# Kernel optimization log

Measured on AMD Instinct MI355X. Metric: run time of the kernel, lower is better.

The kernel has to match this reference:

```python
import jax, jax.numpy as jnp
import numpy as np

# dims
P = 16            # patch size
IMG = 224
D = 768           # embed dim
DEPTH = 12
DI = 1536         # d_inner = expand * D
N = 16            # d_state
DCONV = 4
DTR = 48          # dt_rank = ceil(D / 16)
GS = IMG // P     # 14
L = GS * GS       # 196
KEEP = 49         # (1 - 0.75) * 196
EPS = 1e-5


def _pos2d(embed_dim, gs):
    # replicates get_2d_sincos_pos_embed (numpy, fp32)
    def emb1(ed, pos):
        omega = np.arange(ed // 2, dtype=np.float32) / (ed / 2.0)
        omega = 1.0 / 10000 ** omega
        out = np.einsum('m,d->md', pos.reshape(-1).astype(np.float32), omega)
        return np.concatenate([np.sin(out), np.cos(out)], axis=1)
    gh = np.arange(gs, dtype=np.float32)
    grid = np.meshgrid(gh, gh)  # (w, h) per source
    return np.concatenate([emb1(embed_dim // 2, grid[0]), emb1(embed_dim // 2, grid[1])], axis=1)


def _ln(x, w, b):
    mu = x.mean(-1, keepdims=True)
    var = ((x - mu) ** 2).mean(-1, keepdims=True)
    return (x - mu) * jax.lax.rsqrt(var + EPS) * w + b


def setup_inputs() -> dict:
    key = jax.random.key(0)
    ks = jax.random.split(key, 12)
    s = 0.02
    dt = jnp.exp(jax.random.uniform(ks[7], (DEPTH, DI)) * (np.log(0.1) - np.log(0.001)) + np.log(0.001))
    return {
        'imgs': jax.random.normal(ks[0], (8, 3, IMG, IMG), jnp.float32),
        'noise': jax.random.uniform(ks[1], (8, L), jnp.float32),
        'patch_w': s * jax.random.normal(ks[2], (D, 3, P, P), jnp.float32),
        'patch_b': jnp.zeros((D,), jnp.float32),
        'pos_embed': jnp.asarray(_pos2d(D, GS), jnp.float32),            # [L, D]
        'ln_w': jnp.ones((DEPTH, D), jnp.float32),
        'ln_b': jnp.zeros((DEPTH, D), jnp.float32),
        'in_proj_w': s * jax.random.normal(ks[3], (DEPTH, 2 * DI, D), jnp.float32),
        'conv_w': 0.1 * jax.random.normal(ks[4], (DEPTH, DI, 1, DCONV), jnp.float32),
        'conv_b': jnp.zeros((DEPTH, DI), jnp.float32),
        'x_proj_w': s * jax.random.normal(ks[5], (DEPTH, DTR + 2 * N, DI), jnp.float32),
        'dt_w': s * jax.random.normal(ks[6], (DEPTH, DI, DTR), jnp.float32),
        'dt_b': jnp.log(jnp.expm1(dt)),                                   # inverse softplus
        'A_log': jnp.broadcast_to(jnp.log(jnp.arange(1, N + 1, dtype=jnp.float32)), (DEPTH, DI, N)).copy(),
        'D_skip': jnp.ones((DEPTH, DI), jnp.float32),
        'ssm_ln_w': jnp.ones((DEPTH, DI), jnp.float32),
        'ssm_ln_b': jnp.zeros((DEPTH, DI), jnp.float32),
        'out_proj_w': s * jax.random.normal(ks[8], (DEPTH, D, DI), jnp.float32),
        'final_ln_w': jnp.ones((D,), jnp.float32),
        'final_ln_b': jnp.zeros((D,), jnp.float32),
    }


def _encoder(imgs, noise, patch_w, patch_b, pos_embed, ln_w, ln_b, in_proj_w, conv_w,
             conv_b, x_proj_w, dt_w, dt_b, A_log, D_skip, ssm_ln_w, ssm_ln_b,
             out_proj_w, final_ln_w, final_ln_b):
    B = imgs.shape[0]
    # patch embed: conv stride=kernel=P -> [B, D, 14, 14] -> [B, L, D]
    x = jax.lax.conv_general_dilated(imgs, patch_w, (P, P), 'VALID',
                                     dimension_numbers=('NCHW', 'OIHW', 'NCHW'))
    x = (x + patch_b[None, :, None, None]).reshape(B, D, L).transpose(0, 2, 1)
    x = x + pos_embed[None]

    # random masking (MAE): keep KEEP tokens per sample
    ids_shuffle = jnp.argsort(noise, axis=1)
    ids_restore = jnp.argsort(ids_shuffle, axis=1)
    ids_keep = ids_shuffle[:, :KEEP]
    x = jnp.take_along_axis(x, ids_keep[:, :, None], axis=1)  # [B, KEEP, D]
    mask = jnp.ones((B, L), jnp.float32).at[:, :KEEP].set(0.0)
    mask = jnp.take_along_axis(mask, ids_restore, axis=1)

    def block_step(carry, lp):
        hs, res = carry
        lnw, lnb, ipw, cw, cb, xpw, dtw, dtb, alog, dsk, slw, slb, opw = lp
        res = res + hs                       # Add
        h = _ln(res, lnw, lnb)               # LN
        # --- Mamba mixer ---
        xz = h @ ipw.T                       # [B,K,2*DI]
        xi, z = jnp.split(xz, 2, axis=-1)
        xc = xi.transpose(0, 2, 1)           # [B,DI,K]
        xc = jnp.pad(xc, ((0, 0), (0, 0), (DCONV - 1, 0)))  # causal depthwise conv
        xc = jax.lax.conv_general_dilated(xc, cw, (1,), 'VALID',
                                          dimension_numbers=('NCH', 'OIH', 'NCH'),
                                          feature_group_count=DI)
        xc = jax.nn.silu(xc + cb[None, :, None]).transpose(0, 2, 1)  # [B,K,DI]
        xdbl = xc @ xpw.T                    # [B,K,DTR+2N]
        dtr, Bm, Cm = jnp.split(xdbl, [DTR, DTR + N], axis=-1)
        dt = jax.nn.softplus(dtr @ dtw.T + dtb)      # [B,K,DI]
        A = -jnp.exp(alog)                            # [DI,N]
        dA = jnp.exp(dt[..., None] * A)               # [B,K,DI,N]
        dBx = (dt * xc)[..., None] * Bm[:, :, None, :]
        def scan_step(hstate, inp):
            dA_t, dBx_t, C_t = inp
            hstate = dA_t * hstate + dBx_t            # [B,DI,N]
            y = jnp.einsum('bdn,bn->bd', hstate, C_t)
            return hstate, y
        h0 = jnp.zeros((xc.shape[0], DI, N), xc.dtype)
        _, ys = jax.lax.scan(scan_step, h0,
                             (dA.transpose(1, 0, 2, 3), dBx.transpose(1, 0, 2, 3), Cm.transpose(1, 0, 2)))
        y = ys.transpose(1, 0, 2) + dsk * xc          # D skip
        y = _ln(y, slw, slb)                           # norm after SSM
        y = y * jax.nn.silu(z)                         # gate
        out = y @ opw.T                                # [B,K,D]
        return (out, res), None

    res0 = jnp.zeros_like(x)
    (hs, res), _ = jax.lax.scan(block_step, (x, res0),
                                (ln_w, ln_b, in_proj_w, conv_w, conv_b, x_proj_w, dt_w,
                                 dt_b, A_log, D_skip, ssm_ln_w, ssm_ln_b, out_proj_w))
    latent = _ln(res + hs, final_ln_w, final_ln_b)
    return latent, mask, ids_restore


def reference(imgs, noise, patch_w, patch_b, pos_embed, ln_w, ln_b, in_proj_w, conv_w,
              conv_b, x_proj_w, dt_w, dt_b, A_log, D_skip, ssm_ln_w, ssm_ln_b,
              out_proj_w, final_ln_w, final_ln_b):
    return _encoder(imgs, noise, patch_w, patch_b, pos_embed, ln_w, ln_b, in_proj_w,
                    conv_w, conv_b, x_proj_w, dt_w, dt_b, A_log, D_skip, ssm_ln_w,
                    ssm_ln_b, out_proj_w, final_ln_w, final_ln_b)
```

## Files before the change

### kernel.cpp

```cpp
#include <hip/hip_runtime.h>
#include <cstdint>
#include <cstddef>

namespace {

constexpr int kD    = 768;
constexpr int kDI   = 1536;
constexpr int kN    = 16;
constexpr int kDTR  = 48;
constexpr int kL    = 196;
constexpr int kKeep = 49;
constexpr int kB    = 8;
constexpr int kTok  = kB * kKeep;
constexpr int kPatchRows = kB * kL;
constexpr float kEps = 1e-5f;

typedef __attribute__((ext_vector_type(8))) short short8;
typedef __attribute__((ext_vector_type(4))) float f32x4;

__device__ __forceinline__ short f2bf(float f) {
  unsigned u = __float_as_uint(f);
  return (short)((u + 0x7FFFu + ((u >> 16) & 1u)) >> 16);
}

__device__ __forceinline__ short8 pack8(float4 a, float4 b) {
  short8 r;
  r[0] = f2bf(a.x); r[1] = f2bf(a.y); r[2] = f2bf(a.z); r[3] = f2bf(a.w);
  r[4] = f2bf(b.x); r[5] = f2bf(b.y); r[6] = f2bf(b.z); r[7] = f2bf(b.w);
  return r;
}

__device__ __forceinline__ float block_sum256(float x, float* sbuf) {
#pragma unroll
  for (int o = 32; o > 0; o >>= 1) x += __shfl_down(x, o, 64);
  int wid = threadIdx.x >> 6;
  if ((threadIdx.x & 63) == 0) sbuf[wid] = x;
  __syncthreads();
  float r = sbuf[0] + sbuf[1] + sbuf[2] + sbuf[3];
  __syncthreads();
  return r;
}

__global__ __launch_bounds__(256) void im2col_kernel(const float* __restrict__ imgs,
                                                     float* __restrict__ A2) {
  int idx = blockIdx.x * 256 + threadIdx.x;
  if (idx >= kPatchRows * kD) return;
  int col = idx % kD;
  int row = idx / kD;
  int b = row / kL, l = row % kL;
  int gy = l / 14, gx = l % 14;
  int c   = col >> 8;
  int rem = col & 255;
  int py = rem >> 4, px = rem & 15;
  A2[idx] = imgs[((b * 3 + c) * 224 + gy * 16 + py) * 224 + gx * 16 + px];
}

template <int SPLIT, int ACT, bool KG>
__global__ __launch_bounds__(256) void gemm_mfma(const float* __restrict__ A, int lda,
                                                 const float* __restrict__ W,
                                                 const float* __restrict__ bias,
                                                 float* __restrict__ C, int ldc,
                                                 int M, int N, int K) {
  __shared__ __align__(16) short As[8][64][8];
  __shared__ __align__(16) short Bs[8][64][8];
  const int tid = threadIdx.x;
  const int bm = blockIdx.x * 64;
  const int bn = blockIdx.y * 64;
  const int kc = K / SPLIT;
  const int k0 = blockIdx.z * kc;
  const int nk = (kc + 63) / 64;
  const int sr = tid >> 2;
  const int sq = tid & 3;
  const int lane = tid & 63;
  const int wm = ((tid >> 6) >> 1) * 32;
  const int wn = ((tid >> 6) & 1) * 32;
  const bool mok = (bm + sr) < M;
  const bool nok = (bn + sr) < N;
  const float* Ap = A + (size_t)(bm + sr) * lda + k0 + sq * 16;
  const float* Wp = W + (size_t)(bn + sr) * K + k0 + sq * 16;

  f32x4 acc[2][2];
#pragma unroll
  for (int i = 0; i < 2; ++i)
#pragma unroll
    for (int j = 0; j < 2; ++j) acc[i][j] = (f32x4){0.f, 0.f, 0.f, 0.f};

  for (int kt = 0; kt < nk; ++kt) {
    const int kb = kt * 64;
    const float4 z4 = make_float4(0.f, 0.f, 0.f, 0.f);
    float4 a0 = z4, a1 = z4, a2 = z4, a3 = z4;
    float4 w0 = z4, w1 = z4, w2 = z4, w3 = z4;
    const float* ap = Ap + kb;
    const float* wp = Wp + kb;
    if (!KG) {
      if (mok) {
        a0 = *(const float4*)ap;       a1 = *(const float4*)(ap + 4);
        a2 = *(const float4*)(ap + 8); a3 = *(const float4*)(ap + 12);
      }
      if (nok) {
        w0 = *(const float4*)wp;       w1 = *(const float4*)(wp + 4);
        w2 = *(const float4*)(wp + 8); w3 = *(const float4*)(wp + 12);
      }
    } else {
      const int kq = k0 + kb + sq * 16;
      if (mok) {
        if (kq + 4  <= K) a0 = *(const float4*)ap;
        if (kq + 8  <= K) a1 = *(const float4*)(ap + 4);
        if (kq + 12 <= K) a2 = *(const float4*)(ap + 8);
        if (kq + 16 <= K) a3 = *(const float4*)(ap + 12);
      }
      if (nok) {
        if (kq + 4  <= K) w0 = *(const float4*)wp;
        if (kq + 8  <= K) w1 = *(const float4*)(wp + 4);
        if (kq + 12 <= K) w2 = *(const float4*)(wp + 8);
        if (kq + 16 <= K) w3 = *(const float4*)(wp + 12);
      }
    }
    if (kt) __syncthreads();
    *(short8*)&As[sq * 2][sr][0]     = pack8(a0, a1);
    *(short8*)&As[sq * 2 + 1][sr][0] = pack8(a2, a3);
    *(short8*)&Bs[sq * 2][sr][0]     = pack8(w0, w1);
    *(short8*)&Bs[sq * 2 + 1][sr][0] = pack8(w2, w3);
    __syncthreads();
#pragma unroll
    for (int kh = 0; kh < 2; ++kh) {
      const int kg = kh * 4 + (lane >> 4);
      short8 af0 = *(const short8*)&As[kg][wm + (lane & 15)][0];
      short8 af1 = *(const short8*)&As[kg][wm + 16 + (lane & 15)][0];
      short8 bf0 = *(const short8*)&Bs[kg][wn + (lane & 15)][0];
      short8 bf1 = *(const short8*)&Bs[kg][wn + 16 + (lane & 15)][0];
      acc[0][0] = __builtin_amdgcn_mfma_f32_16x16x32_bf16(af0, bf0, acc[0][0], 0, 0, 0);
      acc[0][1] = __builtin_amdgcn_mfma_f32_16x16x32_bf16(af0, bf1, acc[0][1], 0, 0, 0);
      acc[1][0] = __builtin_amdgcn_mfma_f32_16x16x32_bf16(af1, bf0, acc[1][0], 0, 0, 0);
      acc[1][1] = __builtin_amdgcn_mfma_f32_16x16x32_bf16(af1, bf1, acc[1][1], 0, 0, 0);
    }
  }

  const int mrow = (lane >> 4) * 4;
  const int ncol = lane & 15;
#pragma unroll
  for (int i2 = 0; i2 < 2; ++i2)
#pragma unroll
    for (int j2 = 0; j2 < 2; ++j2) {
      int n = bn + wn + j2 * 16 + ncol;
      if (n >= N) continue;
      float bv = 0.f;
      if (SPLIT == 1) bv = bias ? bias[n] : 0.f;
#pragma unroll
      for (int r = 0; r < 4; ++r) {
        int m = bm + wm + i2 * 16 + mrow + r;
        if (m >= M) continue;
        float v = acc[i2][j2][r];
        if (SPLIT == 1) {
          v += bv;
          if (ACT == 1) v = (v > 20.f) ? v : log1pf(expf(v));
          C[(size_t)m * ldc + n] = v;
        } else {
          C[(size_t)blockIdx.z * ((size_t)M * N) + (size_t)m * N + n] = v;
        }
      }
    }
}

__global__ __launch_bounds__(256) void reduce_kernel(const float* __restrict__ part,
                                                     float* __restrict__ out,
                                                     int total4, int Z) {
  int i = blockIdx.x * 256 + threadIdx.x;
  if (i >= total4) return;
  const float4* p = (const float4*)part;
  float4 s = p[i];
  for (int z = 1; z < Z; ++z) {
    float4 v = p[(size_t)z * total4 + i];
    s.x += v.x; s.y += v.y; s.z += v.z; s.w += v.w;
  }
  ((float4*)out)[i] = s;
}

__global__ __launch_bounds__(256) void sort_kernel(const float* __restrict__ noise,
                                                   int* __restrict__ ids_keep,
                                                   float* __restrict__ mask_out,
                                                   float* __restrict__ idsr_out) {
  __shared__ float nb[kL];
  int b = blockIdx.x;
  int t = threadIdx.x;
  if (t < kL) nb[t] = noise[b * kL + t];
  __syncthreads();
  if (t < kL) {
    float v = nb[t];
    int rank = 0;
    for (int j = 0; j < kL; ++j) {
      float u = nb[j];
      rank += (u < v || (u == v && j < t)) ? 1 : 0;
    }
    if (rank < kKeep) ids_keep[b * kKeep + rank] = t;
    idsr_out[b * kL + t] = (float)rank;
    mask_out[b * kL + t] = (rank < kKeep) ? 0.f : 1.f;
  }
}

__global__ __launch_bounds__(256) void gather_kernel(const float* __restrict__ x0,
                                                     const int* __restrict__ ids_keep,
                                                     const float* __restrict__ pos,
                                                     float* __restrict__ hs) {
  int m = blockIdx.x;
  int b = m / kKeep, k = m % kKeep;
  int l = ids_keep[b * kKeep + k];
  const float* src = x0 + (size_t)(b * kL + l) * kD;
  const float* pp  = pos + (size_t)l * kD;
  float* dst = hs + (size_t)m * kD;
  for (int d = threadIdx.x; d < kD; d += 256) dst[d] = src[d] + pp[d];
}

template <int DD>
__global__ __launch_bounds__(256) void add_ln_kernel(const float* __restrict__ hs,
                                                     float* __restrict__ res,
                                                     const float* __restrict__ w,
                                                     const float* __restrict__ b,
                                                     float* __restrict__ out) {
  constexpr int PT = DD / 256;
  __shared__ float sbuf[4];
  int m = blockIdx.x;
  int t = threadIdx.x;
  float v[PT];
  float s = 0.f;
#pragma unroll
  for (int i = 0; i < PT; ++i) {
    int d = t + i * 256;
    v[i] = res[(size_t)m * DD + d] + hs[(size_t)m * DD + d];
    s += v[i];
  }
  float mean = block_sum256(s, sbuf) * (1.f / DD);
  float s2 = 0.f;
#pragma unroll
  for (int i = 0; i < PT; ++i) { float d0 = v[i] - mean; s2 += d0 * d0; }
  float var = block_sum256(s2, sbuf) * (1.f / DD);
  float rstd = rsqrtf(var + kEps);
#pragma unroll
  for (int i = 0; i < PT; ++i) {
    int d = t + i * 256;
    res[(size_t)m * DD + d] = v[i];
    out[(size_t)m * DD + d] = (v[i] - mean) * rstd * w[d] + b[d];
  }
}

__global__ __launch_bounds__(256) void conv_silu_kernel(const float* __restrict__ xz,
                                                        const float* __restrict__ cw,
                                                        const float* __restrict__ cb,
                                                        float* __restrict__ xc) {
  int idx = blockIdx.x * 256 + threadIdx.x;
  if (idx >= kTok * kDI) return;
  int d  = idx % kDI;
  int mt = idx / kDI;
  int t = mt % kKeep;
  int b = mt / kKeep;
  float acc = cb[d];
#pragma unroll
  for (int k = 0; k < 4; ++k) {
    int tt = t - 3 + k;
    if (tt >= 0) acc += xz[(size_t)(b * kKeep + tt) * 3072 + d] * cw[d * 4 + k];
  }
  xc[idx] = acc / (1.f + expf(-acc));
}

__global__ __launch_bounds__(64) void scan_kernel(const float* __restrict__ dt,
                                                  const float* __restrict__ xc,
                                                  const float* __restrict__ xdbl,
                                                  const float* __restrict__ A_log,
                                                  const float* __restrict__ D_skip,
                                                  float* __restrict__ y) {
  __shared__ float bcs[kKeep][32];
  int d = blockIdx.x * 64 + threadIdx.x;
  int b = blockIdx.y;
  for (int i = threadIdx.x; i < kKeep * 32; i += 64) {
    int t = i >> 5, n = i & 31;
    bcs[t][n] = xdbl[(size_t)(b * kKeep + t) * 80 + kDTR + n];
  }
  __syncthreads();
  float Aloc[kN];
#pragma unroll
  for (int n = 0; n < kN; ++n) Aloc[n] = -expf(A_log[d * kN + n]);
  float dsk = D_skip[d];
  float s[kN];
#pragma unroll
  for (int n = 0; n < kN; ++n) s[n] = 0.f;

  size_t base = (size_t)(b * kKeep) * kDI + d;
  float dtv = dt[base];
  float xcv = xc[base];
  for (int t = 0; t < kKeep; ++t) {
    float dtn = 0.f, xcn = 0.f;
    if (t + 1 < kKeep) {
      dtn = dt[base + (size_t)(t + 1) * kDI];
      xcn = xc[base + (size_t)(t + 1) * kDI];
    }
    float dx = dtv * xcv;
    float yv = 0.f;
#pragma unroll
    for (int n = 0; n < kN; ++n) {
      float sn = expf(dtv * Aloc[n]) * s[n] + dx * bcs[t][n];
      s[n] = sn;
      yv += sn * bcs[t][16 + n];
    }
    y[base + (size_t)t * kDI] = yv + dsk * xcv;
    dtv = dtn; xcv = xcn;
  }
}

__global__ __launch_bounds__(256) void ssm_ln_silu_kernel(const float* __restrict__ y,
                                                          const float* __restrict__ xz,
                                                          const float* __restrict__ w,
                                                          const float* __restrict__ b,
                                                          float* __restrict__ y2) {
  constexpr int PT = kDI / 256;
  __shared__ float sbuf[4];
  int m = blockIdx.x;
  int t = threadIdx.x;
  float v[PT];
  float s = 0.f;
#pragma unroll
  for (int i = 0; i < PT; ++i) {
    int d = t + i * 256;
    v[i] = y[(size_t)m * kDI + d];
    s += v[i];
  }
  float mean = block_sum256(s, sbuf) * (1.f / kDI);
  float s2 = 0.f;
#pragma unroll
  for (int i = 0; i < PT; ++i) { float d0 = v[i] - mean; s2 += d0 * d0; }
  float var = block_sum256(s2, sbuf) * (1.f / kDI);
  float rstd = rsqrtf(var + kEps);
#pragma unroll
  for (int i = 0; i < PT; ++i) {
    int d = t + i * 256;
    float z = xz[(size_t)m * 3072 + kDI + d];
    y2[(size_t)m * kDI + d] =
        ((v[i] - mean) * rstd * w[d] + b[d]) * (z / (1.f + expf(-z)));
  }
}

}

extern "C" void kernel_launch(void* const* d_in, const int* in_sizes, int n_in,
                              void* d_out, int out_size, void* d_ws, size_t ws_size,
                              hipStream_t stream) {
  const float* imgs       = (const float*)d_in[0];
  const float* noise      = (const float*)d_in[1];
  const float* patch_w    = (const float*)d_in[2];
  const float* patch_b    = (const float*)d_in[3];
  const float* pos_embed  = (const float*)d_in[4];
  const float* ln_w       = (const float*)d_in[5];
  const float* ln_b       = (const float*)d_in[6];
  const float* in_proj_w  = (const float*)d_in[7];
  const float* conv_w     = (const float*)d_in[8];
  const float* conv_b     = (const float*)d_in[9];
  const float* x_proj_w   = (const float*)d_in[10];
  const float* dt_w       = (const float*)d_in[11];
  const float* dt_b       = (const float*)d_in[12];
  const float* A_log      = (const float*)d_in[13];
  const float* D_skip     = (const float*)d_in[14];
  const float* ssm_ln_w   = (const float*)d_in[15];
  const float* ssm_ln_b   = (const float*)d_in[16];
  const float* out_proj_w = (const float*)d_in[17];
  const float* final_ln_w = (const float*)d_in[18];
  const float* final_ln_b = (const float*)d_in[19];

  float* out      = (float*)d_out;
  float* latent   = out;
  float* mask_out = out + 301056;
  float* idsr_out = out + 301056 + 1568;

  float* ws   = (float*)d_ws;
  float* hs   = ws;
  float* res  = hs   + 301056;
  float* h    = res  + 301056;
  float* xz   = h    + 301056;
  float* xc   = xz   + 1204224;
  float* xdbl = xc   + 602112;
  float* dtb_ = xdbl + 31360;
  float* ybuf = dtb_ + 602112;
  float* y2   = ybuf + 602112;
  int*   ids_keep = (int*)(y2 + 602112);
  float* A2 = xz;
  float* x0 = xc;
  float* part_xdbl = ybuf;
  float* part_out  = dtb_;

  {
    int tot = kPatchRows * kD;
    im2col_kernel<<<(tot + 255) / 256, 256, 0, stream>>>(imgs, A2);
    gemm_mfma<1, 0, false><<<dim3(25, 12, 1), 256, 0, stream>>>(
        A2, kD, patch_w, patch_b, x0, kD, kPatchRows, kD, kD);
  }

  sort_kernel<<<kB, 256, 0, stream>>>(noise, ids_keep, mask_out, idsr_out);

  gather_kernel<<<kTok, 256, 0, stream>>>(x0, ids_keep, pos_embed, hs);

  hipMemsetAsync(res, 0, (size_t)kTok * kD * sizeof(float), stream);

  for (int l = 0; l < 12; ++l) {
    const float* lnw  = ln_w  + (size_t)l * kD;
    const float* lnb  = ln_b  + (size_t)l * kD;
    const float* ipw  = in_proj_w  + (size_t)l * 2 * kDI * kD;
    const float* cw   = conv_w     + (size_t)l * kDI * 4;
    const float* cb   = conv_b     + (size_t)l * kDI;
    const float* xpw  = x_proj_w   + (size_t)l * (kDTR + 2 * kN) * kDI;
    const float* dtw  = dt_w       + (size_t)l * kDI * kDTR;
    const float* dtbv = dt_b       + (size_t)l * kDI;
    const float* alog = A_log      + (size_t)l * kDI * kN;
    const float* dsk  = D_skip     + (size_t)l * kDI;
    const float* slw  = ssm_ln_w   + (size_t)l * kDI;
    const float* slb  = ssm_ln_b   + (size_t)l * kDI;
    const float* opw  = out_proj_w + (size_t)l * kD * kDI;

    add_ln_kernel<kD><<<kTok, 256, 0, stream>>>(hs, res, lnw, lnb, h);

    gemm_mfma<1, 0, false><<<dim3(7, 48, 1), 256, 0, stream>>>(
        h, kD, ipw, nullptr, xz, 2 * kDI, kTok, 2 * kDI, kD);

    conv_silu_kernel<<<(kTok * kDI + 255) / 256, 256, 0, stream>>>(xz, cw, cb, xc);

    gemm_mfma<24, 0, false><<<dim3(7, 2, 24), 256, 0, stream>>>(
        xc, kDI, xpw, nullptr, part_xdbl, 80, kTok, 80, kDI);
    reduce_kernel<<<(7840 + 255) / 256, 256, 0, stream>>>(part_xdbl, xdbl, 7840, 24);

    gemm_mfma<1, 1, true><<<dim3(7, 24, 1), 256, 0, stream>>>(
        xdbl, 80, dtw, dtbv, dtb_, kDI, kTok, kDI, kDTR);

    scan_kernel<<<dim3(24, kB), 64, 0, stream>>>(dtb_, xc, xdbl, alog, dsk, ybuf);

    ssm_ln_silu_kernel<<<kTok, 256, 0, stream>>>(ybuf, xz, slw, slb, y2);

    gemm_mfma<4, 0, false><<<dim3(7, 12, 4), 256, 0, stream>>>(
        y2, kDI, opw, nullptr, part_out, kD, kTok, kD, kDI);
    reduce_kernel<<<(75264 + 255) / 256, 256, 0, stream>>>(part_out, hs, 75264, 4);
  }

  add_ln_kernel<kD><<<kTok, 256, 0, stream>>>(hs, res, final_ln_w, final_ln_b,
                                              latent);
}
```

Before: 1.600 ms.

## Fuse conv+SiLU into x_proj GEMM, dt_proj into scan, reduce into add-LN

Removes the standalone depthwise conv kernel by recomputing conv+SiLU while loading the x_proj GEMM A tile, and recomputes it again inside the scan. The dt projection and softplus now run per timestep inside the scan kernel, reading dt weights from registers. The out_proj split-K partial sums are reduced inside the next add+LayerNorm instead of a separate reduce kernel. This cuts about three launches per layer and the xc/dt intermediate buffers, at the cost of redundant conv work and heavier per-thread scan work.

```diff
diff --git a/kernel.cpp b/kernel.cpp
--- a/kernel.cpp
+++ b/kernel.cpp
@@ -29,6 +29,8 @@
   r[4] = f2bf(b.x); r[5] = f2bf(b.y); r[6] = f2bf(b.z); r[7] = f2bf(b.w);
   return r;
 }
+
+__device__ __forceinline__ float silu(float x) { return x / (1.f + expf(-x)); }
 
 __device__ __forceinline__ float block_sum256(float x, float* sbuf) {
 #pragma unroll
@@ -55,7 +57,7 @@
   A2[idx] = imgs[((b * 3 + c) * 224 + gy * 16 + py) * 224 + gx * 16 + px];
 }
 
-template <int SPLIT, int ACT, bool KG>
+template <int SPLIT>
 __global__ __launch_bounds__(256) void gemm_mfma(const float* __restrict__ A, int lda,
                                                  const float* __restrict__ W,
                                                  const float* __restrict__ bias,
@@ -68,7 +70,7 @@
   const int bn = blockIdx.y * 64;
   const int kc = K / SPLIT;
   const int k0 = blockIdx.z * kc;
-  const int nk = (kc + 63) / 64;
+  const int nk = kc / 64;
   const int sr = tid >> 2;
   const int sq = tid & 3;
   const int lane = tid & 63;
@@ -92,29 +94,13 @@
     float4 w0 = z4, w1 = z4, w2 = z4, w3 = z4;
     const float* ap = Ap + kb;
     const float* wp = Wp + kb;
-    if (!KG) {
-      if (mok) {
-        a0 = *(const float4*)ap;       a1 = *(const float4*)(ap + 4);
-        a2 = *(const float4*)(ap + 8); a3 = *(const float4*)(ap + 12);
-      }
-      if (nok) {
-        w0 = *(const float4*)wp;       w1 = *(const float4*)(wp + 4);
-        w2 = *(const float4*)(wp + 8); w3 = *(const float4*)(wp + 12);
-      }
-    } else {
-      const int kq = k0 + kb + sq * 16;
-      if (mok) {
-        if (kq + 4  <= K) a0 = *(const float4*)ap;
-        if (kq + 8  <= K) a1 = *(const float4*)(ap + 4);
-        if (kq + 12 <= K) a2 = *(const float4*)(ap + 8);
-        if (kq + 16 <= K) a3 = *(const float4*)(ap + 12);
-      }
-      if (nok) {
-        if (kq + 4  <= K) w0 = *(const float4*)wp;
-        if (kq + 8  <= K) w1 = *(const float4*)(wp + 4);
-        if (kq + 12 <= K) w2 = *(const float4*)(wp + 8);
-        if (kq + 16 <= K) w3 = *(const float4*)(wp + 12);
-      }
+    if (mok) {
+      a0 = *(const float4*)ap;       a1 = *(const float4*)(ap + 4);
+      a2 = *(const float4*)(ap + 8); a3 = *(const float4*)(ap + 12);
+    }
+    if (nok) {
+      w0 = *(const float4*)wp;       w1 = *(const float4*)(wp + 4);
+      w2 = *(const float4*)(wp + 8); w3 = *(const float4*)(wp + 12);
     }
     if (kt) __syncthreads();
     *(short8*)&As[sq * 2][sr][0]     = pack8(a0, a1);
@@ -144,20 +130,117 @@
     for (int j2 = 0; j2 < 2; ++j2) {
       int n = bn + wn + j2 * 16 + ncol;
       if (n >= N) continue;
-      float bv = 0.f;
-      if (SPLIT == 1) bv = bias ? bias[n] : 0.f;
+      float bv = (SPLIT == 1 && bias) ? bias[n] : 0.f;
 #pragma unroll
       for (int r = 0; r < 4; ++r) {
         int m = bm + wm + i2 * 16 + mrow + r;
         if (m >= M) continue;
         float v = acc[i2][j2][r];
         if (SPLIT == 1) {
-          v += bv;
-          if (ACT == 1) v = (v > 20.f) ? v : log1pf(expf(v));
-          C[(size_t)m * ldc + n] = v;
+          C[(size_t)m * ldc + n] = v + bv;
         } else {
           C[(size_t)blockIdx.z * ((size_t)M * N) + (size_t)m * N + n] = v;
         }
+      }
+    }
+}
+
+__global__ __launch_bounds__(256) void gemm_xdbl_conv(const float* __restrict__ xz,
+                                                      const float* __restrict__ cw,
+                                                      const float* __restrict__ cb,
+                                                      const float* __restrict__ W,
+                                                      float* __restrict__ Cpart) {
+  __shared__ __align__(16) short As[8][64][8];
+  __shared__ __align__(16) short Bs[8][64][8];
+  const int tid = threadIdx.x;
+  const int bm = blockIdx.x * 64;
+  const int bn = blockIdx.y * 64;
+  const int k0 = blockIdx.z * 64;
+  const int sr = tid >> 2;
+  const int sq = tid & 3;
+  const int lane = tid & 63;
+  const int wm = ((tid >> 6) >> 1) * 32;
+  const int wn = ((tid >> 6) & 1) * 32;
+  const int m = bm + sr;
+  const bool mok = m < kTok;
+  const bool nok = (bn + sr) < 80;
+  const float4 z4 = make_float4(0.f, 0.f, 0.f, 0.f);
+
+  float4 a[4] = {z4, z4, z4, z4};
+  if (mok) {
+    const int b = m / kKeep, t = m % kKeep;
+    const int dbase = k0 + sq * 16;
+#pragma unroll
+    for (int g = 0; g < 4; ++g) {
+      const int d = dbase + g * 4;
+      float4 cacc = *(const float4*)&cb[d];
+      float4 c0 = *(const float4*)&cw[(d + 0) * 4];
+      float4 c1 = *(const float4*)&cw[(d + 1) * 4];
+      float4 c2 = *(const float4*)&cw[(d + 2) * 4];
+      float4 c3 = *(const float4*)&cw[(d + 3) * 4];
+      const float t0[4] = {c0.x, c0.y, c0.z, c0.w};
+      const float t1[4] = {c1.x, c1.y, c1.z, c1.w};
+      const float t2[4] = {c2.x, c2.y, c2.z, c2.w};
+      const float t3[4] = {c3.x, c3.y, c3.z, c3.w};
+#pragma unroll
+      for (int j = 0; j < 4; ++j) {
+        int tt = t - 3 + j;
+        if (tt < 0) continue;
+        float4 xv = *(const float4*)&xz[(size_t)(b * kKeep + tt) * 3072 + d];
+        cacc.x += xv.x * t0[j];
+        cacc.y += xv.y * t1[j];
+        cacc.z += xv.z * t2[j];
+        cacc.w += xv.w * t3[j];
+      }
+      cacc.x = silu(cacc.x); cacc.y = silu(cacc.y);
+      cacc.z = silu(cacc.z); cacc.w = silu(cacc.w);
+      a[g] = cacc;
+    }
+  }
+  float4 w0 = z4, w1 = z4, w2 = z4, w3 = z4;
+  if (nok) {
+    const float* wp = W + (size_t)(bn + sr) * kDI + k0 + sq * 16;
+    w0 = *(const float4*)wp;       w1 = *(const float4*)(wp + 4);
+    w2 = *(const float4*)(wp + 8); w3 = *(const float4*)(wp + 12);
+  }
+  *(short8*)&As[sq * 2][sr][0]     = pack8(a[0], a[1]);
+  *(short8*)&As[sq * 2 + 1][sr][0] = pack8(a[2], a[3]);
+  *(short8*)&Bs[sq * 2][sr][0]     = pack8(w0, w1);
+  *(short8*)&Bs[sq * 2 + 1][sr][0] = pack8(w2, w3);
+  __syncthreads();
+
+  f32x4 acc[2][2];
+#pragma unroll
+  for (int i = 0; i < 2; ++i)
+#pragma unroll
+    for (int j = 0; j < 2; ++j) acc[i][j] = (f32x4){0.f, 0.f, 0.f, 0.f};
+#pragma unroll
+  for (int kh = 0; kh < 2; ++kh) {
+    const int kg = kh * 4 + (lane >> 4);
+    short8 af0 = *(const short8*)&As[kg][wm + (lane & 15)][0];
+    short8 af1 = *(const short8*)&As[kg][wm + 16 + (lane & 15)][0];
+    short8 bf0 = *(const short8*)&Bs[kg][wn + (lane & 15)][0];
+    short8 bf1 = *(const short8*)&Bs[kg][wn + 16 + (lane & 15)][0];
+    acc[0][0] = __builtin_amdgcn_mfma_f32_16x16x32_bf16(af0, bf0, acc[0][0], 0, 0, 0);
+    acc[0][1] = __builtin_amdgcn_mfma_f32_16x16x32_bf16(af0, bf1, acc[0][1], 0, 0, 0);
+    acc[1][0] = __builtin_amdgcn_mfma_f32_16x16x32_bf16(af1, bf0, acc[1][0], 0, 0, 0);
+    acc[1][1] = __builtin_amdgcn_mfma_f32_16x16x32_bf16(af1, bf1, acc[1][1], 0, 0, 0);
+  }
+
+  const int mrow = (lane >> 4) * 4;
+  const int ncol = lane & 15;
+#pragma unroll
+  for (int i2 = 0; i2 < 2; ++i2)
+#pragma unroll
+    for (int j2 = 0; j2 < 2; ++j2) {
+      int n = bn + wn + j2 * 16 + ncol;
+      if (n >= 80) continue;
+#pragma unroll
+      for (int r = 0; r < 4; ++r) {
+        int mm = bm + wm + i2 * 16 + mrow + r;
+        if (mm >= kTok) continue;
+        Cpart[(size_t)blockIdx.z * (kTok * 80) + (size_t)mm * 80 + n] =
+            acc[i2][j2][r];
       }
     }
 }
@@ -211,8 +294,8 @@
   for (int d = threadIdx.x; d < kD; d += 256) dst[d] = src[d] + pp[d];
 }
 
-template <int DD>
-__global__ __launch_bounds__(256) void add_ln_kernel(const float* __restrict__ hs,
+template <int DD, int NP>
+__global__ __launch_bounds__(256) void add_ln_kernel(const float* __restrict__ part,
                                                      float* __restrict__ res,
                                                      const float* __restrict__ w,
                                                      const float* __restrict__ b,
@@ -226,8 +309,12 @@
 #pragma unroll
   for (int i = 0; i < PT; ++i) {
     int d = t + i * 256;
-    v[i] = res[(size_t)m * DD + d] + hs[(size_t)m * DD + d];
-    s += v[i];
+    float acc = res[(size_t)m * DD + d];
+#pragma unroll
+    for (int z = 0; z < NP; ++z)
+      acc += part[(size_t)z * (kTok * DD) + (size_t)m * DD + d];
+    v[i] = acc;
+    s += acc;
   }
   float mean = block_sum256(s, sbuf) * (1.f / DD);
   float s2 = 0.f;
@@ -243,66 +330,72 @@
   }
 }
 
-__global__ __launch_bounds__(256) void conv_silu_kernel(const float* __restrict__ xz,
-                                                        const float* __restrict__ cw,
-                                                        const float* __restrict__ cb,
-                                                        float* __restrict__ xc) {
-  int idx = blockIdx.x * 256 + threadIdx.x;
-  if (idx >= kTok * kDI) return;
-  int d  = idx % kDI;
-  int mt = idx / kDI;
-  int t = mt % kKeep;
-  int b = mt / kKeep;
-  float acc = cb[d];
-#pragma unroll
-  for (int k = 0; k < 4; ++k) {
-    int tt = t - 3 + k;
-    if (tt >= 0) acc += xz[(size_t)(b * kKeep + tt) * 3072 + d] * cw[d * 4 + k];
-  }
-  xc[idx] = acc / (1.f + expf(-acc));
-}
-
-__global__ __launch_bounds__(64) void scan_kernel(const float* __restrict__ dt,
-                                                  const float* __restrict__ xc,
-                                                  const float* __restrict__ xdbl,
-                                                  const float* __restrict__ A_log,
-                                                  const float* __restrict__ D_skip,
-                                                  float* __restrict__ y) {
+__global__ __launch_bounds__(64) void scan_dt_kernel(const float* __restrict__ xz,
+                                                     const float* __restrict__ xdbl,
+                                                     const float* __restrict__ cw,
+                                                     const float* __restrict__ cb,
+                                                     const float* __restrict__ dtw,
+                                                     const float* __restrict__ dtbv,
+                                                     const float* __restrict__ A_log,
+                                                     const float* __restrict__ D_skip,
+                                                     float* __restrict__ y) {
+  __shared__ __align__(16) float dtr_s[kKeep][kDTR];
   __shared__ float bcs[kKeep][32];
-  int d = blockIdx.x * 64 + threadIdx.x;
-  int b = blockIdx.y;
-  for (int i = threadIdx.x; i < kKeep * 32; i += 64) {
-    int t = i >> 5, n = i & 31;
-    bcs[t][n] = xdbl[(size_t)(b * kKeep + t) * 80 + kDTR + n];
+  const int d0 = blockIdx.x * 64;
+  const int b  = blockIdx.y;
+  const int t  = threadIdx.x;
+  for (int i = t; i < kKeep * 80; i += 64) {
+    int tt = i / 80, c = i % 80;
+    float v = xdbl[(size_t)(b * kKeep + tt) * 80 + c];
+    if (c < kDTR) dtr_s[tt][c] = v;
+    else bcs[tt][c - kDTR] = v;
   }
   __syncthreads();
+
+  const int d = d0 + t;
+  float4 wreg[12];
+#pragma unroll
+  for (int q = 0; q < 12; ++q)
+    wreg[q] = *(const float4*)&dtw[(size_t)d * kDTR + q * 4];
   float Aloc[kN];
 #pragma unroll
-  for (int n = 0; n < kN; ++n) Aloc[n] = -expf(A_log[d * kN + n]);
-  float dsk = D_skip[d];
+  for (int n = 0; n < kN; ++n) Aloc[n] = -expf(A_log[(size_t)d * kN + n]);
+  const float dsk = D_skip[d];
+  const float dtb0 = dtbv[d];
+  const float4 cw4 = *(const float4*)&cw[d * 4];
+  const float cb0 = cb[d];
+
   float s[kN];
 #pragma unroll
   for (int n = 0; n < kN; ++n) s[n] = 0.f;
-
-  size_t base = (size_t)(b * kKeep) * kDI + d;
-  float dtv = dt[base];
-  float xcv = xc[base];
-  for (int t = 0; t < kKeep; ++t) {
-    float dtn = 0.f, xcn = 0.f;
-    if (t + 1 < kKeep) {
-      dtn = dt[base + (size_t)(t + 1) * kDI];
-      xcn = xc[base + (size_t)(t + 1) * kDI];
-    }
+  float w0 = 0.f, w1 = 0.f, w2 = 0.f;
+
+  for (int tt = 0; tt < kKeep; ++tt) {
+    float xin = xz[(size_t)(b * kKeep + tt) * 3072 + d];
+    float cacc = cb0 + w0 * cw4.x + w1 * cw4.y + w2 * cw4.z + xin * cw4.w;
+    w0 = w1; w1 = w2; w2 = xin;
+    float xcv = silu(cacc);
+    float dacc = dtb0;
+#pragma unroll
+    for (int q = 0; q < 12; ++q) {
+      float4 r4 = *(const float4*)&dtr_s[tt][q * 4];
+      dacc += r4.x * wreg[q].x + r4.y * wreg[q].y +
+              r4.z * wreg[q].z + r4.w * wreg[q].w;
+    }
+    float dtv = (dacc > 20.f) ? dacc : log1pf(expf(dacc));
     float dx = dtv * xcv;
+    float4 bc[8];
+#pragma unroll
+    for (int q = 0; q < 8; ++q) bc[q] = *(const float4*)&bcs[tt][q * 4];
+    const float* bf = (const float*)&bc[0];
     float yv = 0.f;
 #pragma unroll
     for (int n = 0; n < kN; ++n) {
-      float sn = expf(dtv * Aloc[n]) * s[n] + dx * bcs[t][n];
+      float sn = expf(dtv * Aloc[n]) * s[n] + dx * bf[n];
       s[n] = sn;
-      yv += sn * bcs[t][16 + n];
-    }
-    y[base + (size_t)t * kDI] = yv + dsk * xcv;
-    dtv = dtn; xcv = xcn;
+      yv += sn * bf[16 + n];
+    }
+    y[(size_t)(b * kKeep + tt) * kDI + d] = yv + dsk * xcv;
   }
 }
 
@@ -334,7 +427,7 @@
     int d = t + i * 256;
     float z = xz[(size_t)m * 3072 + kDI + d];
     y2[(size_t)m * kDI + d] =
-        ((v[i] - mean) * rstd * w[d] + b[d]) * (z / (1.f + expf(-z)));
+        ((v[i] - mean) * rstd * w[d] + b[d]) * silu(z);
   }
 }
 
@@ -369,26 +462,24 @@
   float* mask_out = out + 301056;
   float* idsr_out = out + 301056 + 1568;
 
-  float* ws   = (float*)d_ws;
-  float* hs   = ws;
-  float* res  = hs   + 301056;
-  float* h    = res  + 301056;
-  float* xz   = h    + 301056;
-  float* xc   = xz   + 1204224;
-  float* xdbl = xc   + 602112;
-  float* dtb_ = xdbl + 31360;
-  float* ybuf = dtb_ + 602112;
-  float* y2   = ybuf + 602112;
-  int*   ids_keep = (int*)(y2 + 602112);
+  float* ws        = (float*)d_ws;
+  float* hs        = ws;
+  float* res       = hs + 301056;
+  float* h         = res + 301056;
+  float* xz        = h + 301056;
+  float* xdbl      = xz + 1204224;
+  float* part_xdbl = xdbl + 31360;
+  float* part_out  = part_xdbl + 752640;
+  float* ybuf      = part_out + 1204224;
+  float* y2        = ybuf + 602112;
+  int*   ids_keep  = (int*)(y2 + 602112);
   float* A2 = xz;
-  float* x0 = xc;
-  float* part_xdbl = ybuf;
-  float* part_out  = dtb_;
+  float* x0 = part_xdbl;
 
   {
     int tot = kPatchRows * kD;
     im2col_kernel<<<(tot + 255) / 256, 256, 0, stream>>>(imgs, A2);
-    gemm_mfma<1, 0, false><<<dim3(25, 12, 1), 256, 0, stream>>>(
+    gemm_mfma<1><<<dim3(25, 12, 1), 256, 0, stream>>>(
         A2, kD, patch_w, patch_b, x0, kD, kPatchRows, kD, kD);
   }
 
@@ -413,29 +504,26 @@
     const float* slb  = ssm_ln_b   + (size_t)l * kDI;
     const float* opw  = out_proj_w + (size_t)l * kD * kDI;
 
-    add_ln_kernel<kD><<<kTok, 256, 0, stream>>>(hs, res, lnw, lnb, h);
-
-    gemm_mfma<1, 0, false><<<dim3(7, 48, 1), 256, 0, stream>>>(
+    if (l == 0)
+      add_ln_kernel<kD, 1><<<kTok, 256, 0, stream>>>(hs, res, lnw, lnb, h);
+    else
+      add_ln_kernel<kD, 4><<<kTok, 256, 0, stream>>>(part_out, res, lnw, lnb, h);
+
+    gemm_mfma<1><<<dim3(7, 48, 1), 256, 0, stream>>>(
         h, kD, ipw, nullptr, xz, 2 * kDI, kTok, 2 * kDI, kD);
 
-    conv_silu_kernel<<<(kTok * kDI + 255) / 256, 256, 0, stream>>>(xz, cw, cb, xc);
-
-    gemm_mfma<24, 0, false><<<dim3(7, 2, 24), 256, 0, stream>>>(
-        xc, kDI, xpw, nullptr, part_xdbl, 80, kTok, 80, kDI);
+    gemm_xdbl_conv<<<dim3(7, 2, 24), 256, 0, stream>>>(xz, cw, cb, xpw, part_xdbl);
     reduce_kernel<<<(7840 + 255) / 256, 256, 0, stream>>>(part_xdbl, xdbl, 7840, 24);
 
-    gemm_mfma<1, 1, true><<<dim3(7, 24, 1), 256, 0, stream>>>(
-        xdbl, 80, dtw, dtbv, dtb_, kDI, kTok, kDI, kDTR);
-
-    scan_kernel<<<dim3(24, kB), 64, 0, stream>>>(dtb_, xc, xdbl, alog, dsk, ybuf);
+    scan_dt_kernel<<<dim3(24, kB), 64, 0, stream>>>(xz, xdbl, cw, cb, dtw, dtbv,
+                                                    alog, dsk, ybuf);
 
     ssm_ln_silu_kernel<<<kTok, 256, 0, stream>>>(ybuf, xz, slw, slb, y2);
 
-    gemm_mfma<4, 0, false><<<dim3(7, 12, 4), 256, 0, stream>>>(
+    gemm_mfma<4><<<dim3(7, 12, 4), 256, 0, stream>>>(
         y2, kDI, opw, nullptr, part_out, kD, kTok, kD, kDI);
-    reduce_kernel<<<(75264 + 255) / 256, 256, 0, stream>>>(part_out, hs, 75264, 4);
-  }
-
-  add_ln_kernel<kD><<<kTok, 256, 0, stream>>>(hs, res, final_ln_w, final_ln_b,
-                                              latent);
-}
+  }
+
+  add_ln_kernel<kD, 4><<<kTok, 256, 0, stream>>>(part_out, res, final_ln_w,
+                                                 final_ln_b, latent);
+}
```

New measurement: 1.945 ms. 21.5% more time.
